# Performance work log

Measured on AMD Instinct MI355X. Metric: run time of the kernel, lower is better.

Reference implementation:

```python
import jax, jax.numpy as jnp
import numpy as np

B, S, IN, H, OUT, L = 64, 512, 512, 1024, 512, 2


def setup_inputs() -> dict:
    key = jax.random.key(0)
    ks = jax.random.split(key, 12)
    s_in = 1.0 / np.sqrt(IN)
    s_h = 1.0 / np.sqrt(H)
    inp = {
        "x": jax.random.normal(ks[0], (B, S, IN), dtype=jnp.float32),
        "h0": jnp.zeros((B, L, H), dtype=jnp.float32),
        # layer 0: gates stacked [z; r; g] along first axis
        "Wx0": jax.random.uniform(ks[1], (3 * H, IN), minval=-s_in, maxval=s_in),
        "Wh0": jax.random.uniform(ks[2], (3 * H, H), minval=-s_h, maxval=s_h),
        "bh0": jax.random.uniform(ks[3], (3 * H,), minval=-s_h, maxval=s_h),
        # layer 1 (input dim is H)
        "Wx1": jax.random.uniform(ks[4], (3 * H, H), minval=-s_h, maxval=s_h),
        "Wh1": jax.random.uniform(ks[5], (3 * H, H), minval=-s_h, maxval=s_h),
        "bh1": jax.random.uniform(ks[6], (3 * H,), minval=-s_h, maxval=s_h),
        # output projection fc_hy
        "Why": jax.random.uniform(ks[7], (OUT, H), minval=-s_h, maxval=s_h),
        "by": jax.random.uniform(ks[8], (OUT,), minval=-s_h, maxval=s_h),
    }
    return inp


def _gru_layer(x, h_init, Wx, Wh, bh):
    """x: [B,S,D], h_init: [B,H]. Returns (ys [B,S,H], h_final [B,H])."""
    # Batch the input-side projections for all timesteps at once.
    xp = jnp.einsum("bsd,gd->bsg", x, Wx)  # [B,S,3H]
    xz, xr, xg = jnp.split(xp, 3, axis=-1)
    Whz, Whr, Whg = jnp.split(Wh, 3, axis=0)
    bhz, bhr, bhg = jnp.split(bh, 3, axis=0)

    def step(h, xs):
        xz_t, xr_t, xg_t = xs  # each [B,H]
        z = jax.nn.sigmoid(xz_t + h @ Whz.T + bhz)
        r = jax.nn.sigmoid(xr_t + h @ Whr.T + bhr)
        g = jnp.tanh(xg_t + (r * h) @ Whg.T + bhg)
        h_new = z * h + (1.0 - z) * g
        return h_new, h_new

    # time-major scan
    xs = (xz.transpose(1, 0, 2), xr.transpose(1, 0, 2), xg.transpose(1, 0, 2))
    h_final, ys = jax.lax.scan(step, h_init, xs)
    return ys.transpose(1, 0, 2), h_final  # [B,S,H], [B,H]


def reference(x, h0, Wx0, Wh0, bh0, Wx1, Wh1, bh1, Why, by):
    # dropout rate is 0 -> dropout is identity
    y0, hf0 = _gru_layer(x, h0[:, 0, :], Wx0, Wh0, bh0)
    y1, hf1 = _gru_layer(y0, h0[:, 1, :], Wx1, Wh1, bh1)
    layer_output = jnp.einsum("bsh,oh->bso", y1, Why) + by  # [B,S,OUT]
    hidden_state = jnp.stack([hf0, hf1], axis=1)  # [B,L,H]
    return layer_output, jax.lax.stop_gradient(hidden_state)
```

## Files before the change

### kernel.cpp

```cpp
#include <hip/hip_runtime.h>
#include <hip/hip_bf16.h>

#define B_   64
#define S_   512
#define IN_  512
#define H_   1024
#define OUT_ 512
#define H3_  3072
#define TC_  32
#define TCL2 5
#define NCHUNK (S_ / TC_)
#define MC_  (B_ * TC_)
#define NROW (B_ * S_)

#define NBLK 256
#define NTHR 512
#define EXN  32768
#define FPAD 16
#define STAGE_OFF 0
#define HOWN_OFF  32768
#define ZOWN_OFF  36928
#define SMEM_BYTES 41088

typedef float f32x4 __attribute__((ext_vector_type(4)));
typedef short bf16x8 __attribute__((ext_vector_type(8)));
typedef unsigned int u32;
typedef u32 u32x4 __attribute__((ext_vector_type(4)));

struct ChainArgs {
  const float* xp;
  const __hip_bfloat16* Wh;
  float* hf;
  u32* hbuf;
  u32* rhbuf;
  u32* fA;
  u32* fB;
  __hip_bfloat16* y;
  u32 baseA, baseB;
  int t0;
  int layer;
  int active;
  int stagger;
};

struct GemmTasks {
  const float* x;
  const __hip_bfloat16* wx0;
  const float* bh0;
  float* xp0dst;
  int t0next;
  int xp0_active;
  const __hip_bfloat16* y1src;
  const __hip_bfloat16* why;
  const float* by;
  float* outdst;
  int t0out;
  int out_active;
};

__device__ __forceinline__ u32 f2bf_bits(float v) {
  union { __hip_bfloat16 b; unsigned short s; } cv;
  cv.b = __float2bfloat16(v);
  return (u32)cv.s;
}

__device__ __forceinline__ void coh_st(u32* p, u32 v) {
  __hip_atomic_store(p, v, __ATOMIC_RELAXED, __HIP_MEMORY_SCOPE_AGENT);
}

__device__ __forceinline__ void waitflags(const u32* f, int rgbase, u32 target) {
  const u32* my = f + (size_t)(rgbase + (threadIdx.x & 15)) * FPAD;
  int it = 0;
  while (true) {
    u32 v;
    asm volatile("global_load_dword %0, %1, off sc0 sc1\n\ts_waitcnt vmcnt(0)"
                 : "=v"(v) : "v"(my) : "memory");
    if (__all((int)(v >= target))) break;
    if (it < 2) {
      __builtin_amdgcn_s_sleep(2);
    } else {
      __builtin_amdgcn_s_sleep(8);
    }
    ++it;
  }
  __builtin_amdgcn_sched_barrier(0);
}

__device__ __forceinline__ void stage_ex(const u32* __restrict__ src, char* stage, int tid,
                                         int rg) {
  u32x4 v[4];
#pragma unroll
  for (int i = 0; i < 4; ++i) {
    int c4 = tid + i * NTHR;
    int cgp = c4 >> 7;
    int s = c4 & 127;
    const u32* p = src + (((size_t)(cgp * 4 + rg) * 16 + (s >> 3)) * 32 + (s & 7) * 4);
    asm volatile("global_load_dwordx4 %0, %1, off sc0 sc1" : "=v"(v[i]) : "v"(p));
  }
  asm volatile("s_waitcnt vmcnt(0)" ::: "memory");
#pragma unroll
  for (int i = 0; i < 4; ++i) {
    int c4 = tid + i * NTHR;
    int cgp = c4 >> 7;
    int s = c4 & 127;
    int r = s >> 3;
    *(u32x4*)(stage + r * 2048 + ((cgp * 128 + (s & 7) * 16) ^ ((r & 7) << 4))) = v[i];
  }
}

__global__ __launch_bounds__(256) void cast_f32_to_bf16(const float* __restrict__ in,
                                                        __hip_bfloat16* __restrict__ out,
                                                        int n4) {
  int i = blockIdx.x * 256 + threadIdx.x;
  if (i >= n4) return;
  float4 v = ((const float4*)in)[i];
  out[4 * i + 0] = __float2bfloat16(v.x);
  out[4 * i + 1] = __float2bfloat16(v.y);
  out[4 * i + 2] = __float2bfloat16(v.z);
  out[4 * i + 3] = __float2bfloat16(v.w);
}

__global__ __launch_bounds__(256) void gather_cast_x(const float* __restrict__ x,
                                                     __hip_bfloat16* __restrict__ out, int t0) {
  int i = blockIdx.x * 256 + threadIdx.x;
  int e = i * 4;
  int b = e >> 14;
  int rem = e & 16383;
  float4 v = *(const float4*)(x + (size_t)b * (S_ * IN_) + (size_t)t0 * IN_ + rem);
  out[e + 0] = __float2bfloat16(v.x);
  out[e + 1] = __float2bfloat16(v.y);
  out[e + 2] = __float2bfloat16(v.z);
  out[e + 3] = __float2bfloat16(v.w);
}

template <bool REMAP>
__global__ __launch_bounds__(256) void gemm_nt_bias(const __hip_bfloat16* __restrict__ A,
                                                    const __hip_bfloat16* __restrict__ Bm,
                                                    const float* __restrict__ bias,
                                                    float* __restrict__ C, int M, int N, int K,
                                                    int t0) {
  const int lane = threadIdx.x & 63;
  const int w = threadIdx.x >> 6;
  const int wr = w >> 1, wc = w & 1;
  const int row0 = blockIdx.y * 128 + wr * 64;
  const int col0 = blockIdx.x * 128 + wc * 64;
  const int kl = (lane >> 4) * 8;
  const int m16 = lane & 15;
  f32x4 acc[4][4] = {};
  for (int k0 = 0; k0 < K; k0 += 32) {
    bf16x8 a[4], b[4];
#pragma unroll
    for (int i = 0; i < 4; ++i)
      a[i] = *(const bf16x8*)(A + (size_t)(row0 + i * 16 + m16) * K + k0 + kl);
#pragma unroll
    for (int j = 0; j < 4; ++j)
      b[j] = *(const bf16x8*)(Bm + (size_t)(col0 + j * 16 + m16) * K + k0 + kl);
#pragma unroll
    for (int i = 0; i < 4; ++i)
#pragma unroll
      for (int j = 0; j < 4; ++j)
        acc[i][j] = __builtin_amdgcn_mfma_f32_16x16x32_bf16(a[i], b[j], acc[i][j], 0, 0, 0);
  }
  const int rsub = (lane >> 4) * 4;
#pragma unroll
  for (int i = 0; i < 4; ++i) {
    int row = row0 + i * 16 + rsub;
#pragma unroll
    for (int j = 0; j < 4; ++j) {
      int col = col0 + j * 16 + m16;
      float bv = bias[col];
#pragma unroll
      for (int r = 0; r < 4; ++r) {
        int rr = row + r;
        int crow = REMAP ? ((rr >> TCL2) * S_ + t0 + (rr & (TC_ - 1))) : rr;
        C[(size_t)crow * N + col] = acc[i][j][r] + bv;
      }
    }
  }
}

__device__ void xp0_unit(const GemmTasks& gt, int u, int tl) {
  const int lane = tl & 63;
  const int w = tl >> 6;
  const int wr = w >> 1, wc = w & 1;
  const int row0 = (u & 15) * 128 + wr * 64;
  const int col0 = (u >> 4) * 128 + wc * 64;
  const int kl = (lane >> 4) * 8;
  const int m16 = lane & 15;
  f32x4 acc[4][4] = {};
  for (int k0 = 0; k0 < IN_; k0 += 32) {
    bf16x8 a[4], b[4];
#pragma unroll
    for (int i = 0; i < 4; ++i) {
      int rr = row0 + i * 16 + m16;
      int xrow = (rr >> TCL2) * S_ + gt.t0next + (rr & (TC_ - 1));
      const float* ap = gt.x + (size_t)xrow * IN_ + k0 + kl;
      float4 f0 = *(const float4*)ap;
      float4 f1 = *(const float4*)(ap + 4);
      union { unsigned short s[8]; bf16x8 v; } cv;
      cv.s[0] = (unsigned short)f2bf_bits(f0.x);
      cv.s[1] = (unsigned short)f2bf_bits(f0.y);
      cv.s[2] = (unsigned short)f2bf_bits(f0.z);
      cv.s[3] = (unsigned short)f2bf_bits(f0.w);
      cv.s[4] = (unsigned short)f2bf_bits(f1.x);
      cv.s[5] = (unsigned short)f2bf_bits(f1.y);
      cv.s[6] = (unsigned short)f2bf_bits(f1.z);
      cv.s[7] = (unsigned short)f2bf_bits(f1.w);
      a[i] = cv.v;
    }
#pragma unroll
    for (int j = 0; j < 4; ++j)
      b[j] = *(const bf16x8*)(gt.wx0 + (size_t)(col0 + j * 16 + m16) * IN_ + k0 + kl);
#pragma unroll
    for (int i = 0; i < 4; ++i)
#pragma unroll
      for (int j = 0; j < 4; ++j)
        acc[i][j] = __builtin_amdgcn_mfma_f32_16x16x32_bf16(a[i], b[j], acc[i][j], 0, 0, 0);
  }
  const int rsub = (lane >> 4) * 4;
#pragma unroll
  for (int i = 0; i < 4; ++i) {
    int row = row0 + i * 16 + rsub;
#pragma unroll
    for (int j = 0; j < 4; ++j) {
      int col = col0 + j * 16 + m16;
      float bv = gt.bh0[col];
#pragma unroll
      for (int r = 0; r < 4; ++r)
        gt.xp0dst[(size_t)(row + r) * H3_ + col] = acc[i][j][r] + bv;
    }
  }
}

__device__ void out_unit(const GemmTasks& gt, int u, int tl) {
  const int lane = tl & 63;
  const int w = tl >> 6;
  const int wr = w >> 1, wc = w & 1;
  const int row0 = (u & 15) * 128 + wr * 64;
  const int col0 = (u >> 4) * 128 + wc * 64;
  const int kl = (lane >> 4) * 8;
  const int m16 = lane & 15;
  f32x4 acc[4][4] = {};
  for (int k0 = 0; k0 < H_; k0 += 32) {
    bf16x8 a[4], b[4];
#pragma unroll
    for (int i = 0; i < 4; ++i)
      a[i] = *(const bf16x8*)(gt.y1src + (size_t)(row0 + i * 16 + m16) * H_ + k0 + kl);
#pragma unroll
    for (int j = 0; j < 4; ++j)
      b[j] = *(const bf16x8*)(gt.why + (size_t)(col0 + j * 16 + m16) * H_ + k0 + kl);
#pragma unroll
    for (int i = 0; i < 4; ++i)
#pragma unroll
      for (int j = 0; j < 4; ++j)
        acc[i][j] = __builtin_amdgcn_mfma_f32_16x16x32_bf16(a[i], b[j], acc[i][j], 0, 0, 0);
  }
  const int rsub = (lane >> 4) * 4;
#pragma unroll
  for (int i = 0; i < 4; ++i) {
    int row = row0 + i * 16 + rsub;
#pragma unroll
    for (int j = 0; j < 4; ++j) {
      int col = col0 + j * 16 + m16;
      float bv = gt.by[col];
#pragma unroll
      for (int r = 0; r < 4; ++r) {
        int rr = row + r;
        int crow = (rr >> TCL2) * S_ + gt.t0out + (rr & (TC_ - 1));
        gt.outdst[(size_t)crow * OUT_ + col] = acc[i][j][r] + bv;
      }
    }
  }
}

__device__ void gemm_spare(const GemmTasks& gt) {
  const int gb = (int)blockIdx.x - 128;
  const int h = threadIdx.x >> 8;
  const int tl = threadIdx.x & 255;
  for (int u = gb * 2 + h; u < 448; u += 256) {
    if (u < 384) {
      if (gt.xp0_active) xp0_unit(gt, u, tl);
    } else {
      if (gt.out_active) out_unit(gt, u - 384, tl);
    }
  }
}

__device__ void chain_scan(const ChainArgs& ca, const float* __restrict__ h0,
                           float* __restrict__ hid_out, char* smem, int bx) {
  char* stage = smem + STAGE_OFF;
  float* h_own = (float*)(smem + HOWN_OFF);
  float* z_own = (float*)(smem + ZOWN_OFF);

  const int tid = threadIdx.x;
  const int lane = tid & 63;
  const int w = tid >> 6;
  const int wc = w & 3;
  const int isR = w >> 2;
  const int rg = bx >> 4;
  const int cg = bx & 15;
  const int fid = bx;
  const int rgbase = rg * 16;
  const int m16 = lane & 15;
  const int kl = (lane >> 4) * 8;
  const int rsub = (lane >> 4) * 4;
  const int swzA = (m16 & 7) << 4;
  const int cloc = wc * 16 + m16;

  const float* xp = ca.xp;
  const __hip_bfloat16* Wh = ca.Wh;
  u32* hbuf = ca.hbuf;
  u32* rhbuf = ca.rhbuf;
  u32* flagA = ca.fA;
  u32* flagB = ca.fB;
  const u32 baseA = ca.baseA, baseB = ca.baseB;
  const int t0 = ca.t0, layer = ca.layer;

  for (int i = 0; i < ca.stagger; ++i) __builtin_amdgcn_s_sleep(16);

  {
    int row = tid >> 5, pp = tid & 31;
    int col = cg * 64 + pp * 2;
    int grow = rg * 16 + row;
    float v0, v1;
    if (t0 == 0) {
      v0 = h0[((size_t)grow * 2 + layer) * H_ + col];
      v1 = h0[((size_t)grow * 2 + layer) * H_ + col + 1];
      coh_st(hbuf + EXN + (((size_t)(cg * 4 + rg) * 16 + row) * 32 + pp),
             f2bf_bits(v0) | (f2bf_bits(v1) << 16));
    } else {
      v0 = ca.hf[grow * H_ + col];
      v1 = ca.hf[grow * H_ + col + 1];
    }
    h_own[row * 65 + pp * 2] = v0;
    h_own[row * 65 + pp * 2 + 1] = v1;
  }
  asm volatile("s_waitcnt vmcnt(0)" ::: "memory");
  __syncthreads();
  if (tid == 0) coh_st(flagB + (size_t)fid * FPAD, baseB + 1);

  for (int t = 0; t < TC_; ++t) {
    const int par = t & 1;
    const int colA = cg * 64 + cloc + (isR ? H_ : 0);
    float xpv[4], xpg[4];
#pragma unroll
    for (int j = 0; j < 4; ++j) {
      int grow = rg * 16 + rsub + j;
      xpv[j] = xp[((size_t)(grow * TC_ + t)) * H3_ + colA];
    }
    if (w < 4) {
#pragma unroll
      for (int j = 0; j < 4; ++j) {
        int grow = rg * 16 + rsub + j;
        xpg[j] = xp[((size_t)(grow * TC_ + t)) * H3_ + 2 * H_ + cg * 64 + cloc];
      }
    }

    waitflags(flagB, rgbase, baseB + 1 + t);
    stage_ex(hbuf + (par ^ 1) * EXN, stage, tid, rg);
    __syncthreads();
    {
      f32x4 acc0 = {}, acc1 = {};
      const char* abase = stage + m16 * 2048;
      const __hip_bfloat16* Bb = Wh + (size_t)colA * H_;
#pragma unroll
      for (int k0 = 0; k0 < H_; k0 += 64) {
        bf16x8 a0 = *(const bf16x8*)(abase + (((k0 + kl) * 2) ^ swzA));
        bf16x8 a1 = *(const bf16x8*)(abase + (((k0 + 32 + kl) * 2) ^ swzA));
        bf16x8 b0 = *(const bf16x8*)(Bb + k0 + kl);
        bf16x8 b1 = *(const bf16x8*)(Bb + k0 + 32 + kl);
        acc0 = __builtin_amdgcn_mfma_f32_16x16x32_bf16(a0, b0, acc0, 0, 0, 0);
        acc1 = __builtin_amdgcn_mfma_f32_16x16x32_bf16(a1, b1, acc1, 0, 0, 0);
      }
      if (!isR) {
#pragma unroll
        for (int j = 0; j < 4; ++j) {
          float pre = acc0[j] + acc1[j] + xpv[j];
          z_own[(rsub + j) * 65 + cloc] = 1.f / (1.f + expf(-pre));
        }
      } else {
#pragma unroll
        for (int j = 0; j < 4; ++j) {
          int lr = rsub + j;
          float pre = acc0[j] + acc1[j] + xpv[j];
          float s = 1.f / (1.f + expf(-pre));
          float rh = s * h_own[lr * 65 + cloc];
          u32 bits = f2bf_bits(rh);
          u32 pair = bits | (((u32)__shfl_down((int)bits, 1)) << 16);
          if ((m16 & 1) == 0)
            coh_st(rhbuf + par * EXN + (((size_t)(cg * 4 + rg) * 16 + lr) * 32 + (cloc >> 1)),
                   pair);
        }
        asm volatile("s_waitcnt vmcnt(0)" ::: "memory");
      }
    }
    __syncthreads();
    if (tid == 0) coh_st(flagA + (size_t)fid * FPAD, baseA + t + 1);

    waitflags(flagA, rgbase, baseA + t + 1);
    stage_ex(rhbuf + par * EXN, stage, tid, rg);
    __syncthreads();
    if (w < 4) {
      f32x4 acc0 = {}, acc1 = {};
      const char* abase = stage + m16 * 2048;
      const __hip_bfloat16* Bb = Wh + (size_t)(2 * H_ + cg * 64 + cloc) * H_;
#pragma unroll
      for (int k0 = 0; k0 < H_; k0 += 64) {
        bf16x8 a0 = *(const bf16x8*)(abase + (((k0 + kl) * 2) ^ swzA));
        bf16x8 a1 = *(const bf16x8*)(abase + (((k0 + 32 + kl) * 2) ^ swzA));
        bf16x8 b0 = *(const bf16x8*)(Bb + k0 + kl);
        bf16x8 b1 = *(const bf16x8*)(Bb + k0 + 32 + kl);
        acc0 = __builtin_amdgcn_mfma_f32_16x16x32_bf16(a0, b0, acc0, 0, 0, 0);
        acc1 = __builtin_amdgcn_mfma_f32_16x16x32_bf16(a1, b1, acc1, 0, 0, 0);
      }
#pragma unroll
      for (int j = 0; j < 4; ++j) {
        int lr = rsub + j;
        float pre = acc0[j] + acc1[j] + xpg[j];
        float gg = tanhf(pre);
        float zz = z_own[lr * 65 + cloc];
        float hv = h_own[lr * 65 + cloc];
        float hn = zz * hv + (1.f - zz) * gg;
        h_own[lr * 65 + cloc] = hn;
        u32 bits = f2bf_bits(hn);
        u32 pair = bits | (((u32)__shfl_down((int)bits, 1)) << 16);
        if ((m16 & 1) == 0)
          coh_st(hbuf + par * EXN + (((size_t)(cg * 4 + rg) * 16 + lr) * 32 + (cloc >> 1)), pair);
        ca.y[((size_t)((rg * 16 + lr) * TC_ + t)) * H_ + cg * 64 + cloc] = __float2bfloat16(hn);
      }
      asm volatile("s_waitcnt vmcnt(0)" ::: "memory");
    }
    __syncthreads();
    if (tid == 0) coh_st(flagB + (size_t)fid * FPAD, baseB + t + 2);
  }

  {
    int row = tid >> 5, pp = tid & 31;
    int col = cg * 64 + pp * 2;
    int grow = rg * 16 + row;
    float v0 = h_own[row * 65 + pp * 2];
    float v1 = h_own[row * 65 + pp * 2 + 1];
    ca.hf[grow * H_ + col] = v0;
    ca.hf[grow * H_ + col + 1] = v1;
    if (t0 + TC_ == S_) {
      hid_out[((size_t)grow * 2 + layer) * H_ + col] = v0;
      hid_out[((size_t)grow * 2 + layer) * H_ + col + 1] = v1;
    }
  }
}

__global__ __launch_bounds__(NTHR) void gru_scan_fused(ChainArgs a0, ChainArgs a1,
                                                       const float* __restrict__ h0,
                                                       float* __restrict__ hid_out,
                                                       GemmTasks gt) {
  extern __shared__ char smem[];
  const int bx = blockIdx.x;
  if (bx < 64) {
    if (!a0.active) return;
    chain_scan(a0, h0, hid_out, smem, bx);
  } else if (bx < 128) {
    if (!a1.active) return;
    chain_scan(a1, h0, hid_out, smem, bx - 64);
  } else {
    gemm_spare(gt);
  }
}

extern "C" void kernel_launch(void* const* d_in, const int* in_sizes, int n_in,
                              void* d_out, int out_size, void* d_ws, size_t ws_size,
                              hipStream_t stream) {
  const float* x   = (const float*)d_in[0];
  const float* h0  = (const float*)d_in[1];
  const float* Wx0 = (const float*)d_in[2];
  const float* Wh0 = (const float*)d_in[3];
  const float* bh0 = (const float*)d_in[4];
  const float* Wx1 = (const float*)d_in[5];
  const float* Wh1 = (const float*)d_in[6];
  const float* bh1 = (const float*)d_in[7];
  const float* Why = (const float*)d_in[8];
  const float* by  = (const float*)d_in[9];
  float* out = (float*)d_out;
  float* hid_out = out + (size_t)NROW * OUT_;

  (void)hipFuncSetAttribute((const void*)gru_scan_fused,
                            hipFuncAttributeMaxDynamicSharedMemorySize, SMEM_BYTES);

  char* ws = (char*)d_ws;
  size_t off = 0;
  auto alloc = [&](size_t bytes) {
    char* p = ws + off;
    off += (bytes + 255) & ~(size_t)255;
    return p;
  };
  __hip_bfloat16* wx0b = (__hip_bfloat16*)alloc((size_t)H3_ * IN_ * 2);
  __hip_bfloat16* wh0b = (__hip_bfloat16*)alloc((size_t)H3_ * H_ * 2);
  __hip_bfloat16* wx1b = (__hip_bfloat16*)alloc((size_t)H3_ * H_ * 2);
  __hip_bfloat16* wh1b = (__hip_bfloat16*)alloc((size_t)H3_ * H_ * 2);
  __hip_bfloat16* whyb = (__hip_bfloat16*)alloc((size_t)OUT_ * H_ * 2);
  float* h_f32_0 = (float*)alloc((size_t)B_ * H_ * 4);
  float* h_f32_1 = (float*)alloc((size_t)B_ * H_ * 4);
  u32* hbuf_0  = (u32*)alloc((size_t)2 * EXN * 4);
  u32* hbuf_1  = (u32*)alloc((size_t)2 * EXN * 4);
  u32* rhbuf_0 = (u32*)alloc((size_t)2 * EXN * 4);
  u32* rhbuf_1 = (u32*)alloc((size_t)2 * EXN * 4);
  __hip_bfloat16* x_bfc = (__hip_bfloat16*)alloc((size_t)MC_ * IN_ * 2);
  __hip_bfloat16* y0buf = (__hip_bfloat16*)alloc((size_t)MC_ * H_ * 2);
  __hip_bfloat16* y1buf0 = (__hip_bfloat16*)alloc((size_t)MC_ * H_ * 2);
  __hip_bfloat16* y1buf1 = (__hip_bfloat16*)alloc((size_t)MC_ * H_ * 2);
  float* xp0buf0 = (float*)alloc((size_t)MC_ * H3_ * 4);
  float* xp0buf1 = (float*)alloc((size_t)MC_ * H3_ * 4);
  float* xp1buf  = (float*)alloc((size_t)MC_ * H3_ * 4);
  u32* flags     = (u32*)alloc(4 * 256 * FPAD * 4);
  (void)ws_size;

  (void)hipMemsetAsync(flags, 0, 4 * 256 * FPAD * 4, stream);

  auto cast = [&](const float* in, __hip_bfloat16* o, size_t n) {
    cast_f32_to_bf16<<<dim3((unsigned)((n / 4 + 255) / 256)), dim3(256), 0, stream>>>(in, o,
                                                                                     (int)(n / 4));
  };
  cast(Wx0, wx0b, (size_t)H3_ * IN_);
  cast(Wh0, wh0b, (size_t)H3_ * H_);
  cast(Wx1, wx1b, (size_t)H3_ * H_);
  cast(Wh1, wh1b, (size_t)H3_ * H_);
  cast(Why, whyb, (size_t)OUT_ * H_);

  u32* fA0 = flags;
  u32* fB0 = flags + 256 * FPAD;
  u32* fA1 = flags + 512 * FPAD;
  u32* fB1 = flags + 768 * FPAD;
  float* xp0bufs[2] = {xp0buf0, xp0buf1};
  __hip_bfloat16* y1bufs[2] = {y1buf0, y1buf1};

  auto mkchain = [&](int layer, int chunk, int active) {
    ChainArgs ca;
    int cc = chunk < 0 ? 0 : chunk;
    ca.xp = layer == 0 ? xp0bufs[cc & 1] : xp1buf;
    ca.Wh = layer == 0 ? wh0b : wh1b;
    ca.hf = layer == 0 ? h_f32_0 : h_f32_1;
    ca.hbuf = layer == 0 ? hbuf_0 : hbuf_1;
    ca.rhbuf = layer == 0 ? rhbuf_0 : rhbuf_1;
    ca.fA = layer == 0 ? fA0 : fA1;
    ca.fB = layer == 0 ? fB0 : fB1;
    ca.y = layer == 0 ? y0buf : y1bufs[cc & 1];
    ca.baseA = (u32)cc * TC_;
    ca.baseB = (u32)cc * (TC_ + 1);
    ca.t0 = cc * TC_;
    ca.layer = layer;
    ca.active = active;
    ca.stagger = (layer == 1) ? 14 : 0;
    return ca;
  };

  gather_cast_x<<<dim3(MC_ * IN_ / 4 / 256), dim3(256), 0, stream>>>(x, x_bfc, 0);
  gemm_nt_bias<false><<<dim3(H3_ / 128, MC_ / 128), dim3(256), 0, stream>>>(
      x_bfc, wx0b, bh0, xp0buf0, MC_, H3_, IN_, 0);

  for (int c = 0; c <= NCHUNK; ++c) {
    ChainArgs a0 = mkchain(0, c, c < NCHUNK ? 1 : 0);
    ChainArgs a1 = mkchain(1, c - 1, c > 0 ? 1 : 0);
    GemmTasks gt;
    gt.x = x;
    gt.wx0 = wx0b;
    gt.bh0 = bh0;
    gt.xp0dst = xp0bufs[(c + 1) & 1];
    gt.t0next = (c + 1) * TC_;
    gt.xp0_active = (c + 1 < NCHUNK) ? 1 : 0;
    gt.y1src = y1bufs[c & 1];
    gt.why = whyb;
    gt.by = by;
    gt.outdst = out;
    gt.t0out = (c - 2) * TC_;
    gt.out_active = (c >= 2) ? 1 : 0;
    {
      void* args[] = {(void*)&a0, (void*)&a1, (void*)&h0, (void*)&hid_out, (void*)&gt};
      hipError_t e = hipLaunchCooperativeKernel((void*)gru_scan_fused, dim3(NBLK), dim3(NTHR),
                                                args, SMEM_BYTES, stream);
      if (e != hipSuccess) {
        (void)hipGetLastError();
        gru_scan_fused<<<dim3(NBLK), dim3(NTHR), SMEM_BYTES, stream>>>(a0, a1, h0, hid_out, gt);
      }
    }
    if (c < NCHUNK) {
      gemm_nt_bias<false><<<dim3(H3_ / 128, MC_ / 128), dim3(256), 0, stream>>>(
          y0buf, wx1b, bh1, xp1buf, MC_, H3_, H_, 0);
    }
  }
  gemm_nt_bias<true><<<dim3(OUT_ / 128, MC_ / 128), dim3(256), 0, stream>>>(
      y1bufs[(NCHUNK - 1) & 1], whyb, by, out, MC_, OUT_, H_, (NCHUNK - 1) * TC_);
}
```

Baseline: 9.840 ms.

## Compute layer-1 input projection inside the scan blocks per timestep

```diff
diff --git a/kernel.cpp b/kernel.cpp
--- a/kernel.cpp
+++ b/kernel.cpp
@@ -20,7 +20,8 @@
 #define STAGE_OFF 0
 #define HOWN_OFF  32768
 #define ZOWN_OFF  36928
-#define SMEM_BYTES 41088
+#define XPS_OFF   41088
+#define SMEM_BYTES 53888
 
 typedef float f32x4 __attribute__((ext_vector_type(4)));
 typedef short bf16x8 __attribute__((ext_vector_type(8)));
@@ -36,11 +37,14 @@
   u32* fA;
   u32* fB;
   __hip_bfloat16* y;
+  const __hip_bfloat16* y0src;
+  const __hip_bfloat16* wx1;
+  const float* bh1;
   u32 baseA, baseB;
   int t0;
   int layer;
   int active;
-  int stagger;
+  int selfxp;
 };
 
 struct GemmTasks {
@@ -105,6 +109,35 @@
     int s = c4 & 127;
     int r = s >> 3;
     *(u32x4*)(stage + r * 2048 + ((cgp * 128 + (s & 7) * 16) ^ ((r & 7) << 4))) = v[i];
+  }
+}
+
+__device__ __forceinline__ void compute_xps(const __hip_bfloat16* __restrict__ y0,
+                                            const __hip_bfloat16* __restrict__ wx1,
+                                            const float* __restrict__ bh1,
+                                            float* __restrict__ xps, int rg, int cg, int t,
+                                            int w, int lane) {
+  const int m16 = lane & 15;
+  const int kl = (lane >> 4) * 8;
+  const int rsub = (lane >> 4) * 4;
+  const __hip_bfloat16* Arow = y0 + ((size_t)((rg * 16 + m16) * TC_ + t)) * H_;
+#pragma unroll
+  for (int ti = 0; ti < 2; ++ti) {
+    int tt = w + ti * 8;
+    if (tt >= 12) break;
+    int gate = tt >> 2, sub = tt & 3;
+    int colg = gate * H_ + cg * 64 + sub * 16 + m16;
+    const __hip_bfloat16* Bb = wx1 + (size_t)colg * H_;
+    f32x4 acc = {};
+    for (int k0 = 0; k0 < H_; k0 += 32) {
+      bf16x8 a = *(const bf16x8*)(Arow + k0 + kl);
+      bf16x8 b = *(const bf16x8*)(Bb + k0 + kl);
+      acc = __builtin_amdgcn_mfma_f32_16x16x32_bf16(a, b, acc, 0, 0, 0);
+    }
+    float bv = bh1[colg];
+#pragma unroll
+    for (int r = 0; r < 4; ++r)
+      xps[(rsub + r) * 200 + gate * 64 + sub * 16 + m16] = acc[r] + bv;
   }
 }
 
@@ -291,6 +324,7 @@
   char* stage = smem + STAGE_OFF;
   float* h_own = (float*)(smem + HOWN_OFF);
   float* z_own = (float*)(smem + ZOWN_OFF);
+  float* xps = (float*)(smem + XPS_OFF);
 
   const int tid = threadIdx.x;
   const int lane = tid & 63;
@@ -315,8 +349,7 @@
   u32* flagB = ca.fB;
   const u32 baseA = ca.baseA, baseB = ca.baseB;
   const int t0 = ca.t0, layer = ca.layer;
-
-  for (int i = 0; i < ca.stagger; ++i) __builtin_amdgcn_s_sleep(16);
+  const int selfxp = ca.selfxp;
 
   {
     int row = tid >> 5, pp = tid & 31;
@@ -335,6 +368,7 @@
     h_own[row * 65 + pp * 2] = v0;
     h_own[row * 65 + pp * 2 + 1] = v1;
   }
+  if (selfxp) compute_xps(ca.y0src, ca.wx1, ca.bh1, xps, rg, cg, 0, w, lane);
   asm volatile("s_waitcnt vmcnt(0)" ::: "memory");
   __syncthreads();
   if (tid == 0) coh_st(flagB + (size_t)fid * FPAD, baseB + 1);
@@ -343,16 +377,26 @@
     const int par = t & 1;
     const int colA = cg * 64 + cloc + (isR ? H_ : 0);
     float xpv[4], xpg[4];
-#pragma unroll
-    for (int j = 0; j < 4; ++j) {
-      int grow = rg * 16 + rsub + j;
-      xpv[j] = xp[((size_t)(grow * TC_ + t)) * H3_ + colA];
-    }
-    if (w < 4) {
+    if (selfxp) {
+#pragma unroll
+      for (int j = 0; j < 4; ++j)
+        xpv[j] = xps[(rsub + j) * 200 + (isR ? 64 : 0) + cloc];
+      if (w < 4) {
+#pragma unroll
+        for (int j = 0; j < 4; ++j) xpg[j] = xps[(rsub + j) * 200 + 128 + cloc];
+      }
+    } else {
 #pragma unroll
       for (int j = 0; j < 4; ++j) {
         int grow = rg * 16 + rsub + j;
-        xpg[j] = xp[((size_t)(grow * TC_ + t)) * H3_ + 2 * H_ + cg * 64 + cloc];
+        xpv[j] = xp[((size_t)(grow * TC_ + t)) * H3_ + colA];
+      }
+      if (w < 4) {
+#pragma unroll
+        for (int j = 0; j < 4; ++j) {
+          int grow = rg * 16 + rsub + j;
+          xpg[j] = xp[((size_t)(grow * TC_ + t)) * H3_ + 2 * H_ + cg * 64 + cloc];
+        }
       }
     }
 
@@ -432,6 +476,12 @@
     }
     __syncthreads();
     if (tid == 0) coh_st(flagB + (size_t)fid * FPAD, baseB + t + 2);
+
+    if (selfxp) {
+      if (t + 1 < TC_)
+        compute_xps(ca.y0src, ca.wx1, ca.bh1, xps, rg, cg, t + 1, w, lane);
+      __syncthreads();
+    }
   }
 
   {
@@ -503,13 +553,13 @@
   u32* hbuf_1  = (u32*)alloc((size_t)2 * EXN * 4);
   u32* rhbuf_0 = (u32*)alloc((size_t)2 * EXN * 4);
   u32* rhbuf_1 = (u32*)alloc((size_t)2 * EXN * 4);
-  __hip_bfloat16* x_bfc = (__hip_bfloat16*)alloc((size_t)MC_ * IN_ * 2);
-  __hip_bfloat16* y0buf = (__hip_bfloat16*)alloc((size_t)MC_ * H_ * 2);
+  __hip_bfloat16* x_bfc  = (__hip_bfloat16*)alloc((size_t)MC_ * IN_ * 2);
+  __hip_bfloat16* y0buf0 = (__hip_bfloat16*)alloc((size_t)MC_ * H_ * 2);
+  __hip_bfloat16* y0buf1 = (__hip_bfloat16*)alloc((size_t)MC_ * H_ * 2);
   __hip_bfloat16* y1buf0 = (__hip_bfloat16*)alloc((size_t)MC_ * H_ * 2);
   __hip_bfloat16* y1buf1 = (__hip_bfloat16*)alloc((size_t)MC_ * H_ * 2);
   float* xp0buf0 = (float*)alloc((size_t)MC_ * H3_ * 4);
   float* xp0buf1 = (float*)alloc((size_t)MC_ * H3_ * 4);
-  float* xp1buf  = (float*)alloc((size_t)MC_ * H3_ * 4);
   u32* flags     = (u32*)alloc(4 * 256 * FPAD * 4);
   (void)ws_size;
 
@@ -530,25 +580,29 @@
   u32* fA1 = flags + 512 * FPAD;
   u32* fB1 = flags + 768 * FPAD;
   float* xp0bufs[2] = {xp0buf0, xp0buf1};
+  __hip_bfloat16* y0bufs[2] = {y0buf0, y0buf1};
   __hip_bfloat16* y1bufs[2] = {y1buf0, y1buf1};
 
   auto mkchain = [&](int layer, int chunk, int active) {
     ChainArgs ca;
     int cc = chunk < 0 ? 0 : chunk;
-    ca.xp = layer == 0 ? xp0bufs[cc & 1] : xp1buf;
+    ca.xp = layer == 0 ? xp0bufs[cc & 1] : nullptr;
     ca.Wh = layer == 0 ? wh0b : wh1b;
     ca.hf = layer == 0 ? h_f32_0 : h_f32_1;
     ca.hbuf = layer == 0 ? hbuf_0 : hbuf_1;
     ca.rhbuf = layer == 0 ? rhbuf_0 : rhbuf_1;
     ca.fA = layer == 0 ? fA0 : fA1;
     ca.fB = layer == 0 ? fB0 : fB1;
-    ca.y = layer == 0 ? y0buf : y1bufs[cc & 1];
+    ca.y = layer == 0 ? y0bufs[cc & 1] : y1bufs[cc & 1];
+    ca.y0src = layer == 1 ? y0bufs[cc & 1] : nullptr;
+    ca.wx1 = wx1b;
+    ca.bh1 = bh1;
     ca.baseA = (u32)cc * TC_;
     ca.baseB = (u32)cc * (TC_ + 1);
     ca.t0 = cc * TC_;
     ca.layer = layer;
     ca.active = active;
-    ca.stagger = (layer == 1) ? 14 : 0;
+    ca.selfxp = (layer == 1) ? 1 : 0;
     return ca;
   };
 
@@ -581,10 +635,6 @@
         gru_scan_fused<<<dim3(NBLK), dim3(NTHR), SMEM_BYTES, stream>>>(a0, a1, h0, hid_out, gt);
       }
     }
-    if (c < NCHUNK) {
-      gemm_nt_bias<false><<<dim3(H3_ / 128, MC_ / 128), dim3(256), 0, stream>>>(
-          y0buf, wx1b, bh1, xp1buf, MC_, H3_, H_, 0);
-    }
   }
   gemm_nt_bias<true><<<dim3(OUT_ / 128, MC_ / 128), dim3(256), 0, stream>>>(
       y1bufs[(NCHUNK - 1) & 1], whyb, by, out, MC_, OUT_, H_, (NCHUNK - 1) * TC_);
```

Measured after the change: 19.70 ms. 2x slower.

## Fuse layer-1 input projection into scan kernel with per-timestep readiness counters

Applied to the files above, without the earlier changes.

```diff
diff --git a/kernel.cpp b/kernel.cpp
--- a/kernel.cpp
+++ b/kernel.cpp
@@ -36,11 +36,14 @@
   u32* fA;
   u32* fB;
   __hip_bfloat16* y;
+  u32* xpctr;
+  u32 xptarget;
   u32 baseA, baseB;
   int t0;
   int layer;
   int active;
   int stagger;
+  int xpwait;
 };
 
 struct GemmTasks {
@@ -56,6 +59,12 @@
   float* outdst;
   int t0out;
   int out_active;
+  const __hip_bfloat16* y0src;
+  const __hip_bfloat16* wx1;
+  const float* bh1;
+  float* xp1dst;
+  u32* xpctr;
+  int xp1_active;
 };
 
 __device__ __forceinline__ u32 f2bf_bits(float v) {
@@ -179,6 +188,42 @@
   }
 }
 
+__device__ void xp1_unit(const GemmTasks& gt, int u, int tl) {
+  const int t = u / 24;
+  const int nt = u % 24;
+  const int lane = tl & 63;
+  const int w = tl >> 6;
+  const int m16 = lane & 15;
+  const int kl = (lane >> 4) * 8;
+  const int rsub = (lane >> 4) * 4;
+  const int row0 = w * 16;
+  const __hip_bfloat16* Arow = gt.y0src + ((size_t)((row0 + m16) * TC_ + t)) * H_;
+  f32x4 acc[8] = {};
+  for (int k0 = 0; k0 < H_; k0 += 32) {
+    bf16x8 a = *(const bf16x8*)(Arow + k0 + kl);
+#pragma unroll
+    for (int j = 0; j < 8; ++j) {
+      bf16x8 b = *(const bf16x8*)(gt.wx1 + (size_t)(nt * 128 + j * 16 + m16) * H_ + k0 + kl);
+      acc[j] = __builtin_amdgcn_mfma_f32_16x16x32_bf16(a, b, acc[j], 0, 0, 0);
+    }
+  }
+#pragma unroll
+  for (int j = 0; j < 8; ++j) {
+    int col = nt * 128 + j * 16 + m16;
+    float bv = gt.bh1[col];
+#pragma unroll
+    for (int r = 0; r < 4; ++r) {
+      int row = row0 + rsub + r;
+      coh_st((u32*)(gt.xp1dst + (size_t)(row * TC_ + t) * H3_ + col),
+             __float_as_uint(acc[j][r] + bv));
+    }
+  }
+  asm volatile("s_waitcnt vmcnt(0)" ::: "memory");
+  if (lane == 0)
+    __hip_atomic_fetch_add(gt.xpctr + (size_t)t * FPAD, 1u, __ATOMIC_RELAXED,
+                           __HIP_MEMORY_SCOPE_AGENT);
+}
+
 __device__ void xp0_unit(const GemmTasks& gt, int u, int tl) {
   const int lane = tl & 63;
   const int w = tl >> 6;
@@ -277,11 +322,14 @@
   const int gb = (int)blockIdx.x - 128;
   const int h = threadIdx.x >> 8;
   const int tl = threadIdx.x & 255;
-  for (int u = gb * 2 + h; u < 448; u += 256) {
-    if (u < 384) {
-      if (gt.xp0_active) xp0_unit(gt, u, tl);
+  const int slot = gb * 2 + h;
+  for (int u = slot; u < 1216; u += 256) {
+    if (u < 768) {
+      if (gt.xp1_active) xp1_unit(gt, u, tl);
+    } else if (u < 1152) {
+      if (gt.xp0_active) xp0_unit(gt, u - 768, tl);
     } else {
-      if (gt.out_active) out_unit(gt, u - 384, tl);
+      if (gt.out_active) out_unit(gt, u - 1152, tl);
     }
   }
 }
@@ -343,16 +391,56 @@
     const int par = t & 1;
     const int colA = cg * 64 + cloc + (isR ? H_ : 0);
     float xpv[4], xpg[4];
-#pragma unroll
-    for (int j = 0; j < 4; ++j) {
-      int grow = rg * 16 + rsub + j;
-      xpv[j] = xp[((size_t)(grow * TC_ + t)) * H3_ + colA];
-    }
-    if (w < 4) {
+    if (ca.xpwait) {
+      if (tid < 64) {
+        const u32* cp = ca.xpctr + (size_t)t * FPAD;
+        int it = 0;
+        while (true) {
+          u32 v;
+          asm volatile("global_load_dword %0, %1, off sc0 sc1\n\ts_waitcnt vmcnt(0)"
+                       : "=v"(v) : "v"(cp) : "memory");
+          if (v >= ca.xptarget) break;
+          if (it < 2) {
+            __builtin_amdgcn_s_sleep(2);
+          } else {
+            __builtin_amdgcn_s_sleep(8);
+          }
+          ++it;
+        }
+      }
+      __syncthreads();
+      u32 uv[4], ug[4] = {0, 0, 0, 0};
+#pragma unroll
+      for (int j = 0; j < 4; ++j) {
+        const float* p = xp + ((size_t)((rg * 16 + rsub + j) * TC_ + t)) * H3_ + colA;
+        asm volatile("global_load_dword %0, %1, off sc0 sc1" : "=v"(uv[j]) : "v"(p));
+      }
+      if (w < 4) {
+#pragma unroll
+        for (int j = 0; j < 4; ++j) {
+          const float* p =
+              xp + ((size_t)((rg * 16 + rsub + j) * TC_ + t)) * H3_ + 2 * H_ + cg * 64 + cloc;
+          asm volatile("global_load_dword %0, %1, off sc0 sc1" : "=v"(ug[j]) : "v"(p));
+        }
+      }
+      asm volatile("s_waitcnt vmcnt(0)" ::: "memory");
+#pragma unroll
+      for (int j = 0; j < 4; ++j) {
+        xpv[j] = __uint_as_float(uv[j]);
+        xpg[j] = __uint_as_float(ug[j]);
+      }
+    } else {
 #pragma unroll
       for (int j = 0; j < 4; ++j) {
         int grow = rg * 16 + rsub + j;
-        xpg[j] = xp[((size_t)(grow * TC_ + t)) * H3_ + 2 * H_ + cg * 64 + cloc];
+        xpv[j] = xp[((size_t)(grow * TC_ + t)) * H3_ + colA];
+      }
+      if (w < 4) {
+#pragma unroll
+        for (int j = 0; j < 4; ++j) {
+          int grow = rg * 16 + rsub + j;
+          xpg[j] = xp[((size_t)(grow * TC_ + t)) * H3_ + 2 * H_ + cg * 64 + cloc];
+        }
       }
     }
 
@@ -503,17 +591,20 @@
   u32* hbuf_1  = (u32*)alloc((size_t)2 * EXN * 4);
   u32* rhbuf_0 = (u32*)alloc((size_t)2 * EXN * 4);
   u32* rhbuf_1 = (u32*)alloc((size_t)2 * EXN * 4);
-  __hip_bfloat16* x_bfc = (__hip_bfloat16*)alloc((size_t)MC_ * IN_ * 2);
-  __hip_bfloat16* y0buf = (__hip_bfloat16*)alloc((size_t)MC_ * H_ * 2);
+  __hip_bfloat16* x_bfc  = (__hip_bfloat16*)alloc((size_t)MC_ * IN_ * 2);
+  __hip_bfloat16* y0buf0 = (__hip_bfloat16*)alloc((size_t)MC_ * H_ * 2);
+  __hip_bfloat16* y0buf1 = (__hip_bfloat16*)alloc((size_t)MC_ * H_ * 2);
   __hip_bfloat16* y1buf0 = (__hip_bfloat16*)alloc((size_t)MC_ * H_ * 2);
   __hip_bfloat16* y1buf1 = (__hip_bfloat16*)alloc((size_t)MC_ * H_ * 2);
   float* xp0buf0 = (float*)alloc((size_t)MC_ * H3_ * 4);
   float* xp0buf1 = (float*)alloc((size_t)MC_ * H3_ * 4);
   float* xp1buf  = (float*)alloc((size_t)MC_ * H3_ * 4);
   u32* flags     = (u32*)alloc(4 * 256 * FPAD * 4);
+  u32* xpctr     = (u32*)alloc(32 * FPAD * 4);
   (void)ws_size;
 
   (void)hipMemsetAsync(flags, 0, 4 * 256 * FPAD * 4, stream);
+  (void)hipMemsetAsync(xpctr, 0, 32 * FPAD * 4, stream);
 
   auto cast = [&](const float* in, __hip_bfloat16* o, size_t n) {
     cast_f32_to_bf16<<<dim3((unsigned)((n / 4 + 255) / 256)), dim3(256), 0, stream>>>(in, o,
@@ -530,9 +621,10 @@
   u32* fA1 = flags + 512 * FPAD;
   u32* fB1 = flags + 768 * FPAD;
   float* xp0bufs[2] = {xp0buf0, xp0buf1};
+  __hip_bfloat16* y0bufs[2] = {y0buf0, y0buf1};
   __hip_bfloat16* y1bufs[2] = {y1buf0, y1buf1};
 
-  auto mkchain = [&](int layer, int chunk, int active) {
+  auto mkchain = [&](int layer, int chunk, int active, u32 xptarget) {
     ChainArgs ca;
     int cc = chunk < 0 ? 0 : chunk;
     ca.xp = layer == 0 ? xp0bufs[cc & 1] : xp1buf;
@@ -542,13 +634,16 @@
     ca.rhbuf = layer == 0 ? rhbuf_0 : rhbuf_1;
     ca.fA = layer == 0 ? fA0 : fA1;
     ca.fB = layer == 0 ? fB0 : fB1;
-    ca.y = layer == 0 ? y0buf : y1bufs[cc & 1];
+    ca.y = layer == 0 ? y0bufs[cc & 1] : y1bufs[cc & 1];
+    ca.xpctr = xpctr;
+    ca.xptarget = xptarget;
     ca.baseA = (u32)cc * TC_;
     ca.baseB = (u32)cc * (TC_ + 1);
     ca.t0 = cc * TC_;
     ca.layer = layer;
     ca.active = active;
     ca.stagger = (layer == 1) ? 14 : 0;
+    ca.xpwait = (layer == 1) ? 1 : 0;
     return ca;
   };
 
@@ -557,8 +652,8 @@
       x_bfc, wx0b, bh0, xp0buf0, MC_, H3_, IN_, 0);
 
   for (int c = 0; c <= NCHUNK; ++c) {
-    ChainArgs a0 = mkchain(0, c, c < NCHUNK ? 1 : 0);
-    ChainArgs a1 = mkchain(1, c - 1, c > 0 ? 1 : 0);
+    ChainArgs a0 = mkchain(0, c, c < NCHUNK ? 1 : 0, 0);
+    ChainArgs a1 = mkchain(1, c - 1, c > 0 ? 1 : 0, (u32)c * 96);
     GemmTasks gt;
     gt.x = x;
     gt.wx0 = wx0b;
@@ -572,6 +667,12 @@
     gt.outdst = out;
     gt.t0out = (c - 2) * TC_;
     gt.out_active = (c >= 2) ? 1 : 0;
+    gt.y0src = y0bufs[(c - 1) & 1];
+    gt.wx1 = wx1b;
+    gt.bh1 = bh1;
+    gt.xp1dst = xp1buf;
+    gt.xpctr = xpctr;
+    gt.xp1_active = (c >= 1) ? 1 : 0;
     {
       void* args[] = {(void*)&a0, (void*)&a1, (void*)&h0, (void*)&hid_out, (void*)&gt};
       hipError_t e = hipLaunchCooperativeKernel((void*)gru_scan_fused, dim3(NBLK), dim3(NTHR),
@@ -581,10 +682,6 @@
         gru_scan_fused<<<dim3(NBLK), dim3(NTHR), SMEM_BYTES, stream>>>(a0, a1, h0, hid_out, gt);
       }
     }
-    if (c < NCHUNK) {
-      gemm_nt_bias<false><<<dim3(H3_ / 128, MC_ / 128), dim3(256), 0, stream>>>(
-          y0buf, wx1b, bh1, xp1buf, MC_, H3_, H_, 0);
-    }
   }
   gemm_nt_bias<true><<<dim3(OUT_ / 128, MC_ / 128), dim3(256), 0, stream>>>(
       y1bufs[(NCHUNK - 1) & 1], whyb, by, out, MC_, OUT_, H_, (NCHUNK - 1) * TC_);
```

After: 10.39 ms. +5.6%, slower.
